# Kernel optimization log

Hardware: AMD Instinct MI355X
Metric: run time of the kernel (lower is better)

Reference implementation:

```python
import jax, jax.numpy as jnp
import numpy as np

B, N, D = 2, 1024, 512
H, HD = 8, 64
RPE_IN, RPE_HID = 4, 64
FFN = 2048
EPS = 1e-5


def _layernorm(x, g, b):
    mu = jnp.mean(x, axis=-1, keepdims=True)
    var = jnp.var(x, axis=-1, keepdims=True)
    return (x - mu) * jax.lax.rsqrt(var + EPS) * g + b


def setup_inputs() -> dict:
    key = jax.random.key(0)
    ks = jax.random.split(key, 24)
    s = lambda fan_in: 1.0 / np.sqrt(fan_in)
    # weights stored [in, out] (torch Linear transposed)
    return {
        "x": jax.random.normal(ks[0], (B, N, D), jnp.float32),
        "rel_pos": jax.random.normal(ks[1], (B, N, N, RPE_IN), jnp.float32),
        "Wq": jax.random.uniform(ks[2], (D, D), jnp.float32, -s(D), s(D)),
        "bq": jnp.zeros((D,), jnp.float32),
        "Wk": jax.random.uniform(ks[3], (D, D), jnp.float32, -s(D), s(D)),
        "bk": jnp.zeros((D,), jnp.float32),
        "Wv": jax.random.uniform(ks[4], (D, D), jnp.float32, -s(D), s(D)),
        "bv": jnp.zeros((D,), jnp.float32),
        "Wo": jax.random.uniform(ks[5], (D, D), jnp.float32, -s(D), s(D)),
        "bo": jnp.zeros((D,), jnp.float32),
        "R1": jax.random.uniform(ks[6], (RPE_IN, RPE_HID), jnp.float32, -s(RPE_IN), s(RPE_IN)),
        "rb1": jnp.zeros((RPE_HID,), jnp.float32),
        "R2": jax.random.uniform(ks[7], (RPE_HID, H), jnp.float32, -s(RPE_HID), s(RPE_HID)),
        "rb2": jnp.zeros((H,), jnp.float32),
        "g1": jnp.ones((D,), jnp.float32),
        "b1": jnp.zeros((D,), jnp.float32),
        "g2": jnp.ones((D,), jnp.float32),
        "b2": jnp.zeros((D,), jnp.float32),
        "F1": jax.random.uniform(ks[8], (D, FFN), jnp.float32, -s(D), s(D)),
        "fb1": jnp.zeros((FFN,), jnp.float32),
        "F2": jax.random.uniform(ks[9], (FFN, D), jnp.float32, -s(FFN), s(FFN)),
        "fb2": jnp.zeros((D,), jnp.float32),
    }


def reference(x, rel_pos, Wq, bq, Wk, bk, Wv, bv, Wo, bo,
              R1, rb1, R2, rb2, g1, b1, g2, b2, F1, fb1, F2, fb2):
    scale = 1.0 / np.sqrt(HD)
    q = (x @ Wq + bq).reshape(B, N, H, HD).transpose(0, 2, 1, 3)  # [B,H,N,hd]
    k = (x @ Wk + bk).reshape(B, N, H, HD).transpose(0, 2, 1, 3)
    v = (x @ Wv + bv).reshape(B, N, H, HD).transpose(0, 2, 1, 3)
    attn = jnp.einsum('bhid,bhjd->bhij', q, k) * scale
    rpe = (jax.nn.relu(rel_pos @ R1 + rb1) @ R2 + rb2)  # [B,N,N,H]
    attn = attn + rpe.transpose(0, 3, 1, 2)
    attn = jax.nn.softmax(attn, axis=-1)
    out = jnp.einsum('bhij,bhjd->bhid', attn, v).transpose(0, 2, 1, 3).reshape(B, N, D)
    out = out @ Wo + bo
    x = _layernorm(x + out, g1, b1)
    ffn = jax.nn.gelu(x @ F1 + fb1, approximate=False) @ F2 + fb2
    return _layernorm(x + ffn, g2, b2)
```

## Files before the change

kernel.cpp:

```cpp
#include <hip/hip_runtime.h>
#include <math.h>

#define BATCH 2
#define SEQ   1024
#define DMODEL 512
#define NHEAD 8
#define HDIM  64
#define FFND  2048
#define BH    (BATCH*NHEAD)

typedef float  f32x4   __attribute__((ext_vector_type(4)));
typedef float  f32x16  __attribute__((ext_vector_type(16)));
typedef __bf16 bf16x8  __attribute__((ext_vector_type(8)));

#define WAITVM(n) asm volatile("s_waitcnt vmcnt(" #n ")" ::: "memory")

__device__ __forceinline__ unsigned short f2bf(float f) {
  union { __bf16 h; unsigned short u; } z; z.h = (__bf16)f; return z.u;
}
__device__ __forceinline__ float bf2f(unsigned short h) {
  union { unsigned u; float f; } x; x.u = ((unsigned)h) << 16;
  return x.f;
}
__device__ __forceinline__ unsigned pk2(float a, float b) {
  union { __bf16 h[2]; unsigned u; } z;
  z.h[0] = (__bf16)a; z.h[1] = (__bf16)b; return z.u;
}
__device__ __forceinline__ float gelu_f(float v) {
  float u = 0.7978845608f * (v + 0.044715f * v * v * v);
  float a = fabsf(u);
  float e = __expf(-2.f * a);
  float t = (1.f - e) / (1.f + e);
  t = copysignf(t, u);
  return 0.5f * v * (1.f + t);
}

__device__ __forceinline__ void load_lds16(const void* g, void* l) {
  __builtin_amdgcn_global_load_lds((const __attribute__((address_space(1))) void*)g,
                                   (__attribute__((address_space(3))) void*)l, 16, 0, 0);
}

__global__ __launch_bounds__(256) void prep_misc(
    const float* __restrict__ x, const float* __restrict__ bq,
    const float* __restrict__ bk, const float* __restrict__ bv,
    unsigned short* __restrict__ xb, float* __restrict__ bqkv) {
  int gid = blockIdx.x * 256 + threadIdx.x;
  float4 v = ((const float4*)x)[gid];
  ushort4 s;
  s.x = f2bf(v.x); s.y = f2bf(v.y); s.z = f2bf(v.z); s.w = f2bf(v.w);
  ((ushort4*)xb)[gid] = s;
  if (gid < 1536)
    bqkv[gid] = gid < 512 ? bq[gid] : (gid < 1024 ? bk[gid - 512] : bv[gid - 1024]);
}

__global__ __launch_bounds__(256) void prep_weights(
    const float* __restrict__ Wq, const float* __restrict__ Wk,
    const float* __restrict__ Wv, const float* __restrict__ Wo,
    const float* __restrict__ F1, const float* __restrict__ F2,
    unsigned short* __restrict__ qkvT, unsigned short* __restrict__ WoT,
    unsigned short* __restrict__ F1T, unsigned short* __restrict__ F2T) {
  __shared__ float t[32][33];
  int bid = blockIdx.x;
  const float* src; unsigned short* dst; int R, C, tx, ty;
  if (bid < 1024) {
    int m = bid >> 8;
    src = m == 0 ? Wq : m == 1 ? Wk : m == 2 ? Wv : Wo;
    dst = m < 3 ? qkvT + m * 512 * 512 : WoT;
    R = 512; C = 512; int u = bid & 255; tx = u & 15; ty = u >> 4;
  } else if (bid < 2048) {
    src = F1; dst = F1T; R = 512; C = 2048;
    int u = bid - 1024; tx = u & 63; ty = u >> 6;
  } else {
    src = F2; dst = F2T; R = 2048; C = 512;
    int u = bid - 2048; tx = u & 15; ty = u >> 4;
  }
  int c0 = tx * 32, r0 = ty * 32;
  int x_ = threadIdx.x, y_ = threadIdx.y;
#pragma unroll
  for (int i = 0; i < 4; i++)
    t[y_ + i * 8][x_] = src[(size_t)(r0 + y_ + i * 8) * C + c0 + x_];
  __syncthreads();
#pragma unroll
  for (int i = 0; i < 4; i++)
    dst[(size_t)(c0 + y_ + i * 8) * R + r0 + x_] = f2bf(t[x_][y_ + i * 8]);
}

__global__ __launch_bounds__(256) void rpe_mfma(
    const float* __restrict__ rel, const float* __restrict__ R1,
    const float* __restrict__ rb1, const float* __restrict__ R2,
    const float* __restrict__ rb2, unsigned short* __restrict__ rpe) {
  __shared__ unsigned short Hs[4][32 * 64];
  __shared__ unsigned short Os[4][8 * 32];
  const int tid = threadIdx.x, lane = tid & 63, w = tid >> 6;
  const int l31 = lane & 31, hi = lane >> 5;
  const int l15 = lane & 15, l4g = lane >> 4;
  char* Hw = (char*)&Hs[w][0];
  char* Ow = (char*)&Os[w][0];

  bf16x8 a1[2];
#pragma unroll
  for (int mt = 0; mt < 2; mt++) {
    bf16x8 z = {};
    if (hi == 0) {
      int d = mt * 32 + l31;
      z[0] = (__bf16)R1[0 * 64 + d];
      z[1] = (__bf16)R1[1 * 64 + d];
      z[2] = (__bf16)R1[2 * 64 + d];
      z[3] = (__bf16)R1[3 * 64 + d];
      z[4] = (__bf16)rb1[d];
    }
    a1[mt] = z;
  }
  bf16x8 b2f[2];
#pragma unroll
  for (int ks = 0; ks < 2; ks++) {
    bf16x8 z = {};
    if (l15 < 8) {
#pragma unroll
      for (int j = 0; j < 8; j++)
        z[j] = (__bf16)R2[(ks * 32 + l4g * 8 + j) * 8 + l15];
    }
    b2f[ks] = z;
  }
  float rb2v = (l15 < 8) ? rb2[l15] : 0.f;

  const int wgid = blockIdx.x * 4 + w;
  for (int c = 0; c < 8; c++) {
    int p0 = (wgid + c * 8192) * 32;
    bf16x8 b1 = {};
    if (hi == 0) {
      float4 rv = *(const float4*)&rel[(size_t)(p0 + l31) * 4];
      b1[0] = (__bf16)rv.x; b1[1] = (__bf16)rv.y;
      b1[2] = (__bf16)rv.z; b1[3] = (__bf16)rv.w;
      b1[4] = (__bf16)1.0f;
    }
#pragma unroll
    for (int mt = 0; mt < 2; mt++) {
      f32x16 hz = {};
      f32x16 h = __builtin_amdgcn_mfma_f32_32x32x16_bf16(a1[mt], b1, hz, 0, 0, 0);
#pragma unroll
      for (int q = 0; q < 4; q++) {
        float v0 = fmaxf(h[4 * q + 0], 0.f), v1 = fmaxf(h[4 * q + 1], 0.f);
        float v2 = fmaxf(h[4 * q + 2], 0.f), v3 = fmaxf(h[4 * q + 3], 0.f);
        uint2 pk; pk.x = pk2(v0, v1); pk.y = pk2(v2, v3);
        int byte = (l31 * 128 + (mt * 32 + q * 8 + hi * 4) * 2) ^ ((l31 & 7) << 4);
        *(uint2*)(Hw + byte) = pk;
      }
    }
    f32x4 acc2[2];
    acc2[0] = (f32x4){0.f, 0.f, 0.f, 0.f};
    acc2[1] = (f32x4){0.f, 0.f, 0.f, 0.f};
#pragma unroll
    for (int ks = 0; ks < 2; ks++)
#pragma unroll
      for (int mt2 = 0; mt2 < 2; mt2++) {
        int row = mt2 * 16 + l15;
        int byte = (row * 128 + (ks * 32 + l4g * 8) * 2) ^ ((row & 7) << 4);
        bf16x8 af = *(const bf16x8*)(Hw + byte);
        acc2[mt2] = __builtin_amdgcn_mfma_f32_16x16x32_bf16(af, b2f[ks], acc2[mt2], 0, 0, 0);
      }
#pragma unroll
    for (int mt2 = 0; mt2 < 2; mt2++) {
      if (l15 < 8) {
        uint2 pk;
        pk.x = pk2(acc2[mt2][0] + rb2v, acc2[mt2][1] + rb2v);
        pk.y = pk2(acc2[mt2][2] + rb2v, acc2[mt2][3] + rb2v);
        int byte = l15 * 64 + (mt2 * 16 + l4g * 4) * 2;
        *(uint2*)(Ow + byte) = pk;
      }
    }
    {
      int h = lane >> 3, j0 = (lane & 7) * 4;
      uint2 ov = *(const uint2*)(Ow + h * 64 + j0 * 2);
      int b = p0 >> 20, ij0 = (p0 & 1048575) + j0;
      *(uint2*)&rpe[((size_t)(b * 8 + h) << 20) + ij0] = ov;
    }
  }
}

enum { EPI_F32 = 0, EPI_GELU = 1, EPI_QKV = 2 };

template <int EPI, int BMt, int BNt, int WM, int WN>
__global__ __launch_bounds__(256) void gemm_bt(
    const unsigned short* __restrict__ A, const unsigned short* __restrict__ Bt,
    const float* __restrict__ bias, void* __restrict__ O0, void* __restrict__ O1,
    void* __restrict__ O2, int M, int N, int K) {
  __shared__ unsigned short As[2][BMt * 64];
  __shared__ unsigned short Bs[2][BNt * 64];
  const int tid = threadIdx.x, lane = tid & 63, w = tid >> 6;
  const int wr = w >> 1, wc = w & 1;
  const int m0 = blockIdx.y * BMt, n0 = blockIdx.x * BNt;
  const int l15 = lane & 15, l4g = lane >> 4;
  constexpr int NL = BMt / 32 + BNt / 32;

  f32x4 acc[WM][WN];
#pragma unroll
  for (int i = 0; i < WM; i++)
#pragma unroll
    for (int j = 0; j < WN; j++) acc[i][j] = (f32x4){0.f, 0.f, 0.f, 0.f};

  auto stage = [&](int buf, int kt) {
#pragma unroll
    for (int it = 0; it < BMt / 32; ++it) {
      int c = it * 256 + tid, row = c >> 3;
      int s16 = (c & 7) ^ (row & 7);
      load_lds16(A + (size_t)(m0 + row) * K + kt * 64 + s16 * 8,
                 (char*)&As[buf][0] + c * 16);
    }
#pragma unroll
    for (int it = 0; it < BNt / 32; ++it) {
      int c = it * 256 + tid, row = c >> 3;
      int s16 = (c & 7) ^ (row & 7);
      load_lds16(Bt + (size_t)(n0 + row) * K + kt * 64 + s16 * 8,
                 (char*)&Bs[buf][0] + c * 16);
    }
  };

  const int nkt = K / 64;
  stage(0, 0);
  for (int kt = 0; kt < nkt; ++kt) {
    const int cur = kt & 1;
    if (kt + 1 < nkt) {
      stage(cur ^ 1, kt + 1);
      if constexpr (NL == 6) WAITVM(6); else WAITVM(4);
    } else {
      WAITVM(0);
    }
    __builtin_amdgcn_s_barrier();
#pragma unroll
    for (int kk = 0; kk < 2; ++kk) {
      bf16x8 af[WM], bfv[WN];
#pragma unroll
      for (int i = 0; i < WM; i++) {
        int row = wr * (WM * 16) + i * 16 + l15;
        af[i] = *(const bf16x8*)((char*)&As[cur][0] + row * 128 +
                                 (((kk * 4 + l4g) ^ (row & 7)) << 4));
      }
#pragma unroll
      for (int j = 0; j < WN; j++) {
        int row = wc * (WN * 16) + j * 16 + l15;
        bfv[j] = *(const bf16x8*)((char*)&Bs[cur][0] + row * 128 +
                                  (((kk * 4 + l4g) ^ (row & 7)) << 4));
      }
#pragma unroll
      for (int i = 0; i < WM; i++)
#pragma unroll
        for (int j = 0; j < WN; j++)
          acc[i][j] = __builtin_amdgcn_mfma_f32_16x16x32_bf16(af[i], bfv[j], acc[i][j], 0, 0, 0);
    }
    if (kt + 1 < nkt) {
      asm volatile("" ::: "memory");
      __builtin_amdgcn_s_barrier();
    }
  }

#pragma unroll
  for (int i = 0; i < WM; i++) {
    int row = m0 + wr * (WM * 16) + i * 16 + l4g * 4;
#pragma unroll
    for (int j = 0; j < WN; j++) {
      int col = n0 + wc * (WN * 16) + j * 16 + l15;
      float bv = bias ? bias[col] : 0.f;
#pragma unroll
      for (int r = 0; r < 4; r++) {
        float v = acc[i][j][r] + bv;
        int rr = row + r;
        if (EPI == EPI_F32) {
          ((float*)O0)[(size_t)rr * N + col] = v;
        } else if (EPI == EPI_GELU) {
          ((unsigned short*)O0)[(size_t)rr * N + col] = f2bf(gelu_f(v));
        } else {
          int b = rr >> 10, n = rr & 1023;
          int d = col & 511, h = d >> 6, hd = d & 63;
          int bh = b * 8 + h;
          unsigned short bv16 = f2bf(v);
          if (col < 512)
            ((unsigned short*)O0)[((size_t)bh * 1024 + n) * 64 + hd] = bv16;
          else if (col < 1024)
            ((unsigned short*)O1)[((size_t)bh * 1024 + n) * 64 + hd] = bv16;
          else
            ((unsigned short*)O2)[((size_t)bh * 64 + hd) * 1024 + n] = bv16;
        }
      }
    }
  }
}

__global__ __launch_bounds__(256) void attn_kernel(
    const unsigned short* __restrict__ Qh, const unsigned short* __restrict__ Kh,
    const unsigned short* __restrict__ VT, const unsigned short* __restrict__ rpe,
    unsigned short* __restrict__ AO) {
  __shared__ unsigned short Ks[2][64 * 64], Vs[2][64 * 64], Rs[2][64 * 64];
  __shared__ unsigned short Ps[4][16 * 64];
  const int tid = threadIdx.x, lane = tid & 63, w = tid >> 6;
  const int l15 = lane & 15, l4g = lane >> 4;
  const int bid = blockIdx.x;
  const int it = (bid >> 3) & 15;
  const int bh = (bid & 7) | ((bid >> 7) << 3);
  const int i0 = it * 64;
  const unsigned short* Qb = Qh + (size_t)bh * SEQ * HDIM;
  const unsigned short* Kb = Kh + (size_t)bh * SEQ * HDIM;
  const unsigned short* Vb = VT + (size_t)bh * HDIM * SEQ;
  const unsigned short* Rb = rpe + ((size_t)bh << 20);

  bf16x8 qf[2];
#pragma unroll
  for (int kk = 0; kk < 2; kk++)
    qf[kk] = *(const bf16x8*)&Qb[(size_t)(i0 + w * 16 + l15) * 64 + kk * 32 + l4g * 8];

  f32x4 o[4];
#pragma unroll
  for (int i = 0; i < 4; i++) o[i] = (f32x4){0.f, 0.f, 0.f, 0.f};
  float m4[4], l4s[4];
#pragma unroll
  for (int r = 0; r < 4; r++) { m4[r] = -1e30f; l4s[r] = 0.f; }

  auto stage = [&](int buf, int jt) {
    int j0 = jt * 64;
#pragma unroll
    for (int itn = 0; itn < 2; ++itn) {
      int c = itn * 256 + tid, row = c >> 3;
      int s8 = ((c & 7) ^ (row & 7)) * 8;
      load_lds16(Kb + (size_t)(j0 + row) * 64 + s8, (char*)&Ks[buf][0] + c * 16);
      load_lds16(Vb + (size_t)row * SEQ + j0 + s8, (char*)&Vs[buf][0] + c * 16);
      load_lds16(Rb + (size_t)(i0 + row) * SEQ + j0 + s8, (char*)&Rs[buf][0] + c * 16);
    }
  };

  stage(0, 0);
  for (int jt = 0; jt < 16; ++jt) {
    const int cur = jt & 1;
    if (jt < 15) {
      stage(cur ^ 1, jt + 1);
      WAITVM(6);
    } else {
      WAITVM(0);
    }
    __builtin_amdgcn_s_barrier();

    f32x4 sa[4];
#pragma unroll
    for (int js = 0; js < 4; js++) sa[js] = (f32x4){0.f, 0.f, 0.f, 0.f};
    __builtin_amdgcn_s_setprio(1);
#pragma unroll
    for (int kk = 0; kk < 2; kk++) {
#pragma unroll
      for (int js = 0; js < 4; js++) {
        int row = js * 16 + l15;
        bf16x8 kb = *(const bf16x8*)((char*)&Ks[cur][0] + row * 128 +
                                     (((kk * 4 + l4g) ^ (row & 7)) << 4));
        sa[js] = __builtin_amdgcn_mfma_f32_16x16x32_bf16(qf[kk], kb, sa[js], 0, 0, 0);
      }
    }
    __builtin_amdgcn_s_setprio(0);
    float p[4][4], mx[4];
#pragma unroll
    for (int r = 0; r < 4; r++) mx[r] = -1e30f;
#pragma unroll
    for (int js = 0; js < 4; js++)
#pragma unroll
      for (int r = 0; r < 4; r++) {
        int row = w * 16 + l4g * 4 + r;
        int byte = row * 128 + ((((js * 2) + (l15 >> 3)) ^ (row & 7)) << 4) + ((l15 & 7) << 1);
        float rv = bf2f(*(const unsigned short*)((const char*)&Rs[cur][0] + byte));
        float s = sa[js][r] * 0.125f + rv;
        p[js][r] = s;
        mx[r] = fmaxf(mx[r], s);
      }
#pragma unroll
    for (int off = 1; off < 16; off <<= 1)
#pragma unroll
      for (int r = 0; r < 4; r++) mx[r] = fmaxf(mx[r], __shfl_xor(mx[r], off));
    float al[4], sm[4];
#pragma unroll
    for (int r = 0; r < 4; r++) {
      float nm = fmaxf(m4[r], mx[r]);
      al[r] = __expf(m4[r] - nm);
      m4[r] = nm;
      sm[r] = 0.f;
    }
#pragma unroll
    for (int js = 0; js < 4; js++)
#pragma unroll
      for (int r = 0; r < 4; r++) {
        float e = __expf(p[js][r] - m4[r]);
        p[js][r] = e;
        sm[r] += e;
      }
#pragma unroll
    for (int off = 1; off < 16; off <<= 1)
#pragma unroll
      for (int r = 0; r < 4; r++) sm[r] += __shfl_xor(sm[r], off);
#pragma unroll
    for (int r = 0; r < 4; r++) l4s[r] = l4s[r] * al[r] + sm[r];
#pragma unroll
    for (int hdf = 0; hdf < 4; hdf++)
#pragma unroll
      for (int r = 0; r < 4; r++) o[hdf][r] *= al[r];
#pragma unroll
    for (int js = 0; js < 4; js++)
#pragma unroll
      for (int r = 0; r < 4; r++) {
        int row = l4g * 4 + r;
        int byte = row * 128 + ((((js * 2) + (l15 >> 3)) ^ (row & 7)) << 4) + ((l15 & 7) << 1);
        *(unsigned short*)((char*)&Ps[w][0] + byte) = f2bf(p[js][r]);
      }
    __builtin_amdgcn_s_setprio(1);
#pragma unroll
    for (int kk = 0; kk < 2; kk++) {
      bf16x8 pf = *(const bf16x8*)((char*)&Ps[w][0] + l15 * 128 +
                                   (((kk * 4 + l4g) ^ (l15 & 7)) << 4));
#pragma unroll
      for (int hdf = 0; hdf < 4; hdf++) {
        int row = hdf * 16 + l15;
        bf16x8 vb = *(const bf16x8*)((char*)&Vs[cur][0] + row * 128 +
                                     (((kk * 4 + l4g) ^ (row & 7)) << 4));
        o[hdf] = __builtin_amdgcn_mfma_f32_16x16x32_bf16(pf, vb, o[hdf], 0, 0, 0);
      }
    }
    __builtin_amdgcn_s_setprio(0);
    if (jt < 15) {
      asm volatile("" ::: "memory");
      __builtin_amdgcn_s_barrier();
    }
  }
  const int b = bh >> 3, h = bh & 7;
#pragma unroll
  for (int hdf = 0; hdf < 4; hdf++)
#pragma unroll
    for (int r = 0; r < 4; r++) {
      float v = o[hdf][r] / l4s[r];
      int n = i0 + w * 16 + l4g * 4 + r;
      AO[((size_t)b * SEQ + n) * DMODEL + h * 64 + hdf * 16 + l15] = f2bf(v);
    }
}

__global__ __launch_bounds__(256) void ln_kernel(
    const float* __restrict__ a, const float* __restrict__ res,
    const float* __restrict__ g, const float* __restrict__ be,
    float* __restrict__ outf, unsigned short* __restrict__ outb) {
  const int row = blockIdx.x, t = threadIdx.x;
  const float* pa = a + (size_t)row * DMODEL;
  const float* pb = res + (size_t)row * DMODEL;
  float v0 = pa[t] + pb[t];
  float v1 = pa[t + 256] + pb[t + 256];
  float s = v0 + v1, sq = v0 * v0 + v1 * v1;
#pragma unroll
  for (int off = 1; off < 64; off <<= 1) {
    s += __shfl_xor(s, off);
    sq += __shfl_xor(sq, off);
  }
  __shared__ float ls[4], lq[4];
  int w = t >> 6, lane = t & 63;
  if (lane == 0) { ls[w] = s; lq[w] = sq; }
  __syncthreads();
  s = ls[0] + ls[1] + ls[2] + ls[3];
  sq = lq[0] + lq[1] + lq[2] + lq[3];
  float mu = s * (1.f / DMODEL);
  float var = sq * (1.f / DMODEL) - mu * mu;
  float rs = rsqrtf(var + 1e-5f);
  float y0 = (v0 - mu) * rs * g[t] + be[t];
  float y1v = (v1 - mu) * rs * g[t + 256] + be[t + 256];
  outf[(size_t)row * DMODEL + t] = y0;
  outf[(size_t)row * DMODEL + t + 256] = y1v;
  if (outb) {
    outb[(size_t)row * DMODEL + t] = f2bf(y0);
    outb[(size_t)row * DMODEL + t + 256] = f2bf(y1v);
  }
}

extern "C" void kernel_launch(void* const* d_in, const int* in_sizes, int n_in,
                              void* d_out, int out_size, void* d_ws, size_t ws_size,
                              hipStream_t stream) {
  const float* x   = (const float*)d_in[0];
  const float* rel = (const float*)d_in[1];
  const float* Wq  = (const float*)d_in[2];
  const float* bq  = (const float*)d_in[3];
  const float* Wk  = (const float*)d_in[4];
  const float* bk  = (const float*)d_in[5];
  const float* Wv  = (const float*)d_in[6];
  const float* bv  = (const float*)d_in[7];
  const float* Wo  = (const float*)d_in[8];
  const float* bo  = (const float*)d_in[9];
  const float* R1  = (const float*)d_in[10];
  const float* rb1 = (const float*)d_in[11];
  const float* R2  = (const float*)d_in[12];
  const float* rb2 = (const float*)d_in[13];
  const float* g1  = (const float*)d_in[14];
  const float* b1  = (const float*)d_in[15];
  const float* g2  = (const float*)d_in[16];
  const float* b2  = (const float*)d_in[17];
  const float* F1  = (const float*)d_in[18];
  const float* fb1 = (const float*)d_in[19];
  const float* F2  = (const float*)d_in[20];
  const float* fb2 = (const float*)d_in[21];

  char* p = (char*)d_ws;
  auto alloc = [&](size_t bytes) {
    char* r = p;
    p += (bytes + 255) & ~(size_t)255;
    return r;
  };
  unsigned short* xb   = (unsigned short*)alloc((size_t)2048 * 512 * 2);
  unsigned short* qkvT = (unsigned short*)alloc((size_t)1536 * 512 * 2);
  float*          bqkv = (float*)alloc(1536 * 4);
  unsigned short* WoT  = (unsigned short*)alloc((size_t)512 * 512 * 2);
  unsigned short* F1T  = (unsigned short*)alloc((size_t)2048 * 512 * 2);
  unsigned short* F2T  = (unsigned short*)alloc((size_t)512 * 2048 * 2);
  unsigned short* Qhp  = (unsigned short*)alloc((size_t)BH * SEQ * HDIM * 2);
  unsigned short* Khp  = (unsigned short*)alloc((size_t)BH * SEQ * HDIM * 2);
  unsigned short* VTp  = (unsigned short*)alloc((size_t)BH * HDIM * SEQ * 2);
  unsigned short* rpep = (unsigned short*)alloc((size_t)BH * SEQ * SEQ * 2);
  unsigned short* attO = (unsigned short*)alloc((size_t)2048 * 512 * 2);
  float*          t1   = (float*)alloc((size_t)2048 * 512 * 4);
  float*          y1   = (float*)alloc((size_t)2048 * 512 * 4);
  unsigned short* y1b  = (unsigned short*)alloc((size_t)2048 * 512 * 2);
  float*          t2   = t1;
  unsigned short* hbuf = rpep;

  prep_misc<<<1024, 256, 0, stream>>>(x, bq, bk, bv, xb, bqkv);
  prep_weights<<<3072, dim3(32, 8), 0, stream>>>(Wq, Wk, Wv, Wo, F1, F2,
                                                 qkvT, WoT, F1T, F2T);
  rpe_mfma<<<2048, 256, 0, stream>>>(rel, R1, rb1, R2, rb2, rpep);

  gemm_bt<EPI_QKV, 128, 64, 4, 2><<<dim3(24, 16), 256, 0, stream>>>(
      xb, qkvT, bqkv, Qhp, Khp, VTp, 2048, 1536, 512);
  attn_kernel<<<256, 256, 0, stream>>>(Qhp, Khp, VTp, rpep, attO);

  gemm_bt<EPI_F32, 64, 64, 2, 2><<<dim3(8, 32), 256, 0, stream>>>(
      attO, WoT, bo, t1, nullptr, nullptr, 2048, 512, 512);
  ln_kernel<<<2048, 256, 0, stream>>>(x, t1, g1, b1, y1, y1b);

  gemm_bt<EPI_GELU, 128, 64, 4, 2><<<dim3(32, 16), 256, 0, stream>>>(
      y1b, F1T, fb1, hbuf, nullptr, nullptr, 2048, 2048, 512);
  gemm_bt<EPI_F32, 64, 64, 2, 2><<<dim3(8, 32), 256, 0, stream>>>(
      hbuf, F2T, fb2, t2, nullptr, nullptr, 2048, 512, 2048);
  ln_kernel<<<2048, 256, 0, stream>>>(y1, t2, g2, b2, (float*)d_out, nullptr);
}
```

Measured before the change: 245.4 us.

## Split attention into 32-row blocks and streamline RPE kernel stores and loads

The attention kernel now runs 512 blocks of 128 threads, each covering 32 query rows instead of 64. This doubles grid parallelism on a 256-CU device, and the staging loops and wait counts are adjusted to match. The RPE kernel prefetches the next rel_pos chunk one iteration ahead and uses a new XOR swizzle on its hidden-activation LDS tile. It also writes results straight to global memory, dropping the LDS transpose buffer. In exchange, K/V tiles are loaded twice as often overall, and the direct RPE stores are narrower and less coalesced.

```diff
diff --git a/kernel.cpp b/kernel.cpp
--- a/kernel.cpp
+++ b/kernel.cpp
@@ -90,12 +90,10 @@
     const float* __restrict__ rb1, const float* __restrict__ R2,
     const float* __restrict__ rb2, unsigned short* __restrict__ rpe) {
   __shared__ unsigned short Hs[4][32 * 64];
-  __shared__ unsigned short Os[4][8 * 32];
   const int tid = threadIdx.x, lane = tid & 63, w = tid >> 6;
   const int l31 = lane & 31, hi = lane >> 5;
   const int l15 = lane & 15, l4g = lane >> 4;
   char* Hw = (char*)&Hs[w][0];
-  char* Ow = (char*)&Os[w][0];
 
   bf16x8 a1[2];
 #pragma unroll
@@ -125,15 +123,22 @@
   float rb2v = (l15 < 8) ? rb2[l15] : 0.f;
 
   const int wgid = blockIdx.x * 4 + w;
+  float4 rv = {};
+  if (hi == 0) rv = *(const float4*)&rel[(size_t)(wgid * 32 + l31) * 4];
+
   for (int c = 0; c < 8; c++) {
     int p0 = (wgid + c * 8192) * 32;
+    float4 rc = rv;
+    if (c < 7 && hi == 0)
+      rv = *(const float4*)&rel[(size_t)((wgid + (c + 1) * 8192) * 32 + l31) * 4];
+
     bf16x8 b1 = {};
     if (hi == 0) {
-      float4 rv = *(const float4*)&rel[(size_t)(p0 + l31) * 4];
-      b1[0] = (__bf16)rv.x; b1[1] = (__bf16)rv.y;
-      b1[2] = (__bf16)rv.z; b1[3] = (__bf16)rv.w;
+      b1[0] = (__bf16)rc.x; b1[1] = (__bf16)rc.y;
+      b1[2] = (__bf16)rc.z; b1[3] = (__bf16)rc.w;
       b1[4] = (__bf16)1.0f;
     }
+    const int g1w = ((l31 & 7) ^ (l31 >> 3)) << 4;
 #pragma unroll
     for (int mt = 0; mt < 2; mt++) {
       f32x16 hz = {};
@@ -143,7 +148,7 @@
         float v0 = fmaxf(h[4 * q + 0], 0.f), v1 = fmaxf(h[4 * q + 1], 0.f);
         float v2 = fmaxf(h[4 * q + 2], 0.f), v3 = fmaxf(h[4 * q + 3], 0.f);
         uint2 pk; pk.x = pk2(v0, v1); pk.y = pk2(v2, v3);
-        int byte = (l31 * 128 + (mt * 32 + q * 8 + hi * 4) * 2) ^ ((l31 & 7) << 4);
+        int byte = (l31 * 128 + mt * 64 + q * 16 + hi * 8) ^ g1w;
         *(uint2*)(Hw + byte) = pk;
       }
     }
@@ -151,29 +156,26 @@
     acc2[0] = (f32x4){0.f, 0.f, 0.f, 0.f};
     acc2[1] = (f32x4){0.f, 0.f, 0.f, 0.f};
 #pragma unroll
-    for (int ks = 0; ks < 2; ks++)
-#pragma unroll
-      for (int mt2 = 0; mt2 < 2; mt2++) {
-        int row = mt2 * 16 + l15;
-        int byte = (row * 128 + (ks * 32 + l4g * 8) * 2) ^ ((row & 7) << 4);
+    for (int mt2 = 0; mt2 < 2; mt2++) {
+      int row = mt2 * 16 + l15;
+      int gr = ((row & 7) ^ (row >> 3)) << 4;
+#pragma unroll
+      for (int ks = 0; ks < 2; ks++) {
+        int byte = row * 128 + (((ks * 4 + l4g) << 4) ^ gr);
         bf16x8 af = *(const bf16x8*)(Hw + byte);
         acc2[mt2] = __builtin_amdgcn_mfma_f32_16x16x32_bf16(af, b2f[ks], acc2[mt2], 0, 0, 0);
       }
-#pragma unroll
-    for (int mt2 = 0; mt2 < 2; mt2++) {
-      if (l15 < 8) {
+    }
+    if (l15 < 8) {
+      int b = p0 >> 20, ij0 = (p0 & 1048575);
+      size_t base = ((size_t)(b * 8 + l15) << 20) + ij0;
+#pragma unroll
+      for (int mt2 = 0; mt2 < 2; mt2++) {
         uint2 pk;
         pk.x = pk2(acc2[mt2][0] + rb2v, acc2[mt2][1] + rb2v);
         pk.y = pk2(acc2[mt2][2] + rb2v, acc2[mt2][3] + rb2v);
-        int byte = l15 * 64 + (mt2 * 16 + l4g * 4) * 2;
-        *(uint2*)(Ow + byte) = pk;
-      }
-    }
-    {
-      int h = lane >> 3, j0 = (lane & 7) * 4;
-      uint2 ov = *(const uint2*)(Ow + h * 64 + j0 * 2);
-      int b = p0 >> 20, ij0 = (p0 & 1048575) + j0;
-      *(uint2*)&rpe[((size_t)(b * 8 + h) << 20) + ij0] = ov;
+        *(uint2*)&rpe[base + mt2 * 16 + l4g * 4] = pk;
+      }
     }
   }
 }
@@ -286,18 +288,19 @@
   }
 }
 
-__global__ __launch_bounds__(256) void attn_kernel(
+__global__ __launch_bounds__(128) void attn_kernel(
     const unsigned short* __restrict__ Qh, const unsigned short* __restrict__ Kh,
     const unsigned short* __restrict__ VT, const unsigned short* __restrict__ rpe,
     unsigned short* __restrict__ AO) {
-  __shared__ unsigned short Ks[2][64 * 64], Vs[2][64 * 64], Rs[2][64 * 64];
-  __shared__ unsigned short Ps[4][16 * 64];
+  __shared__ unsigned short Ks[2][64 * 64], Vs[2][64 * 64];
+  __shared__ unsigned short Rs[2][32 * 64];
+  __shared__ unsigned short Ps[2][16 * 64];
   const int tid = threadIdx.x, lane = tid & 63, w = tid >> 6;
   const int l15 = lane & 15, l4g = lane >> 4;
   const int bid = blockIdx.x;
-  const int it = (bid >> 3) & 15;
-  const int bh = (bid & 7) | ((bid >> 7) << 3);
-  const int i0 = it * 64;
+  const int it = (bid >> 3) & 31;
+  const int bh = (bid & 7) | (((bid >> 8) & 1) << 3);
+  const int i0 = it * 32;
   const unsigned short* Qb = Qh + (size_t)bh * SEQ * HDIM;
   const unsigned short* Kb = Kh + (size_t)bh * SEQ * HDIM;
   const unsigned short* Vb = VT + (size_t)bh * HDIM * SEQ;
@@ -318,11 +321,21 @@
   auto stage = [&](int buf, int jt) {
     int j0 = jt * 64;
 #pragma unroll
-    for (int itn = 0; itn < 2; ++itn) {
-      int c = itn * 256 + tid, row = c >> 3;
+    for (int itn = 0; itn < 4; ++itn) {
+      int c = itn * 128 + tid, row = c >> 3;
       int s8 = ((c & 7) ^ (row & 7)) * 8;
       load_lds16(Kb + (size_t)(j0 + row) * 64 + s8, (char*)&Ks[buf][0] + c * 16);
+    }
+#pragma unroll
+    for (int itn = 0; itn < 4; ++itn) {
+      int c = itn * 128 + tid, row = c >> 3;
+      int s8 = ((c & 7) ^ (row & 7)) * 8;
       load_lds16(Vb + (size_t)row * SEQ + j0 + s8, (char*)&Vs[buf][0] + c * 16);
+    }
+#pragma unroll
+    for (int itn = 0; itn < 2; ++itn) {
+      int c = itn * 128 + tid, row = c >> 3;
+      int s8 = ((c & 7) ^ (row & 7)) * 8;
       load_lds16(Rb + (size_t)(i0 + row) * SEQ + j0 + s8, (char*)&Rs[buf][0] + c * 16);
     }
   };
@@ -332,7 +345,7 @@
     const int cur = jt & 1;
     if (jt < 15) {
       stage(cur ^ 1, jt + 1);
-      WAITVM(6);
+      WAITVM(10);
     } else {
       WAITVM(0);
     }
@@ -525,7 +538,7 @@
 
   gemm_bt<EPI_QKV, 128, 64, 4, 2><<<dim3(24, 16), 256, 0, stream>>>(
       xb, qkvT, bqkv, Qhp, Khp, VTp, 2048, 1536, 512);
-  attn_kernel<<<256, 256, 0, stream>>>(Qhp, Khp, VTp, rpep, attO);
+  attn_kernel<<<512, 128, 0, stream>>>(Qhp, Khp, VTp, rpep, attO);
 
   gemm_bt<EPI_F32, 64, 64, 2, 2><<<dim3(8, 32), 256, 0, stream>>>(
       attO, WoT, bo, t1, nullptr, nullptr, 2048, 512, 512);
```

Result: no change. 248.4 us (+1.2%).
